# Optimization experiments

Hardware: AMD Instinct MI355X
Metric: run time of the kernel (lower is better)

Reference implementation:

```python
import jax, jax.numpy as jnp
import numpy as np

D_MODEL = 1024
N_HEADS = 16
LN_EPS = 1e-6  # flax LayerNorm default

def setup_inputs() -> dict:
    key = jax.random.key(0)
    k1, k2, k3 = jax.random.split(key, 3)
    B, S = 2, 2048
    x = jax.random.normal(k1, (B, S, D_MODEL), dtype=jnp.float32)
    W_qkv = jax.random.normal(k2, (D_MODEL, 3 * D_MODEL), dtype=jnp.float32) / np.sqrt(D_MODEL)
    W_out = jax.random.normal(k3, (D_MODEL, D_MODEL), dtype=jnp.float32) / np.sqrt(D_MODEL)
    q_scale = jnp.ones((D_MODEL,), dtype=jnp.float32)
    k_scale = jnp.ones((D_MODEL,), dtype=jnp.float32)
    return {"x": x, "W_qkv": W_qkv, "q_scale": q_scale, "k_scale": k_scale, "W_out": W_out}

def _layernorm(t, scale):
    mu = jnp.mean(t, axis=-1, keepdims=True)
    var = jnp.var(t, axis=-1, keepdims=True)
    return (t - mu) * jax.lax.rsqrt(var + LN_EPS) * scale

def reference(x, W_qkv, q_scale, k_scale, W_out):
    B, S, D = x.shape
    H = N_HEADS
    Hd = D // H
    # fused QKV projection (no bias)
    qkv = jnp.einsum('bsd,de->bse', x, W_qkv)
    q, k, v = jnp.split(qkv, 3, axis=-1)
    # QK-LayerNorm over full d_model (before head split), scale only
    q = _layernorm(q, q_scale)
    k = _layernorm(k, k_scale)
    # split heads: [b, s, h, hd]
    q = q.reshape(B, S, H, Hd)
    k = k.reshape(B, S, H, Hd)
    v = v.reshape(B, S, H, Hd)
    # eager attention with causal mask
    scores = jnp.einsum('bshd,bthd->bhst', q / jnp.sqrt(Hd).astype(q.dtype), k)  # [b,h,s,t]
    future = jnp.triu(jnp.ones((S, S), dtype=bool), 1)  # True on strictly-future positions
    scores = jnp.where(future[None, None, :, :], jnp.finfo(scores.dtype).min, scores)
    attn = jax.nn.softmax(scores, axis=-1)
    ctx = jnp.einsum('bhst,bthd->bshd', attn, v)
    out = jnp.einsum('bsd,de->bse', ctx.reshape(B, S, D), W_out)
    return out
```

## Files before the change

kernel.cpp:

```cpp
#include <hip/hip_runtime.h>
#include <cstdint>
#include <cstddef>

typedef __attribute__((ext_vector_type(8))) short short8;
typedef __attribute__((ext_vector_type(4))) float floatx4;

__device__ __forceinline__ float bf2f(unsigned short u) {
  union { unsigned int i; float f; } c; c.i = ((unsigned int)u) << 16; return c.f;
}
__device__ __forceinline__ unsigned short f2bf(float f) {
  union { float f; unsigned int i; } c; c.f = f;
  unsigned int r = c.i + 0x7fffu + ((c.i >> 16) & 1u);
  return (unsigned short)(r >> 16);
}
__device__ __forceinline__ unsigned int fbits(float f) {
  union { float f; unsigned int i; } c; c.f = f; return c.i;
}

__device__ __forceinline__ void glds16(const unsigned short* g, unsigned short* l) {
  __builtin_amdgcn_global_load_lds((const __attribute__((address_space(1))) void*)g,
                                   (__attribute__((address_space(3))) void*)l, 16, 0, 0);
}

__device__ __forceinline__ void tr_tile(const float* __restrict__ in,
                                        unsigned short* __restrict__ out,
                                        int R, int C, int bx, int by, int tid,
                                        unsigned short (*t)[33]) {
  const int cx = tid & 31, rl = tid >> 5;
#pragma unroll
  for (int i = 0; i < 4; ++i)
    t[rl + i * 8][cx] = f2bf(in[(size_t)(by * 32 + rl + i * 8) * C + bx * 32 + cx]);
  __syncthreads();
  const int oc = by * 32 + cx;
#pragma unroll
  for (int i = 0; i < 4; ++i)
    out[(size_t)(bx * 32 + rl + i * 8) * R + oc] = t[cx][rl + i * 8];
}

__global__ __launch_bounds__(256) void k_prep(const float* __restrict__ x,
                                              const float* __restrict__ Wq,
                                              const float* __restrict__ Wo,
                                              unsigned short* __restrict__ x_bf,
                                              unsigned short* __restrict__ WTq,
                                              unsigned short* __restrict__ WTo) {
  __shared__ unsigned short t[32][33];
  const int bid = blockIdx.x, tid = threadIdx.x;
  if (bid < 3072) {
    tr_tile(Wq, WTq, 1024, 3072, bid % 96, bid / 96, tid, t);
  } else if (bid < 4096) {
    int v = bid - 3072;
    tr_tile(Wo, WTo, 1024, 1024, v & 31, v >> 5, tid, t);
  } else {
    int i = (bid - 4096) * 256 + tid;
    float4 v = ((const float4*)x)[i];
    ushort4 o = { f2bf(v.x), f2bf(v.y), f2bf(v.z), f2bf(v.w) };
    ((ushort4*)x_bf)[i] = o;
  }
}

template <int MT, bool F32OUT>
__global__ __launch_bounds__(256) void k_gemm_bt(const unsigned short* __restrict__ A,
                                                 const unsigned short* __restrict__ BT,
                                                 void* __restrict__ Cout,
                                                 int M, int N, int K) {
  constexpr int NI = MT / 32;
  __shared__ unsigned short As[MT * 32];
  __shared__ unsigned short Bs[128 * 32];
  const int bm = blockIdx.x * MT, bn = blockIdx.y * 128;
  const int tid = threadIdx.x;
  const int wave = tid >> 6, lane = tid & 63;
  const int wm = (wave & 1) * (MT / 2), wn = (wave >> 1) * 64;
  const int lrow = lane & 15, lgrp = lane >> 4;
  floatx4 acc[NI][4] = {};

  const int lr4 = lane >> 2, lc8 = (lane & 3) * 8;
  const int br0 = wave * 32;
  const unsigned short* Bg0 = BT + (size_t)(bn + br0 + lr4) * K + lc8;
  const unsigned short* Bg1 = BT + (size_t)(bn + br0 + 16 + lr4) * K + lc8;
  unsigned short* lB0 = &Bs[br0 * 32];
  unsigned short* lB1 = &Bs[(br0 + 16) * 32];
  const int ar0 = wave * (MT / 4);
  const unsigned short* Ag0 = A + (size_t)(bm + ar0 + lr4) * K + lc8;
  const unsigned short* Ag1 = A + (size_t)(bm + ar0 + 16 + lr4) * K + lc8;
  unsigned short* lA0 = &As[ar0 * 32];
  unsigned short* lA1 = &As[(ar0 + 16) * 32];

  for (int k0 = 0; k0 < K; k0 += 32) {
    glds16(Ag0 + k0, lA0);
    if (MT == 128) glds16(Ag1 + k0, lA1);
    glds16(Bg0 + k0, lB0);
    glds16(Bg1 + k0, lB1);
    __syncthreads();
    short8 a[NI], bfr[4];
#pragma unroll
    for (int i = 0; i < NI; ++i)
      a[i] = *(const short8*)&As[(wm + i * 16 + lrow) * 32 + lgrp * 8];
#pragma unroll
    for (int j = 0; j < 4; ++j)
      bfr[j] = *(const short8*)&Bs[(wn + j * 16 + lrow) * 32 + lgrp * 8];
#pragma unroll
    for (int i = 0; i < NI; ++i)
#pragma unroll
      for (int j = 0; j < 4; ++j)
        acc[i][j] = __builtin_amdgcn_mfma_f32_16x16x32_bf16(a[i], bfr[j], acc[i][j], 0, 0, 0);
    __syncthreads();
  }
#pragma unroll
  for (int i = 0; i < NI; ++i)
#pragma unroll
    for (int j = 0; j < 4; ++j)
#pragma unroll
      for (int r = 0; r < 4; ++r) {
        int m = bm + wm + i * 16 + lgrp * 4 + r;
        int n = bn + wn + j * 16 + lrow;
        if (F32OUT)
          ((float*)Cout)[(size_t)m * N + n] = acc[i][j][r];
        else
          ((unsigned short*)Cout)[(size_t)m * N + n] = f2bf(acc[i][j][r]);
      }
}

__global__ __launch_bounds__(256) void k_lnv(const unsigned short* __restrict__ qkv,
                                             const float* __restrict__ q_scale,
                                             const float* __restrict__ k_scale,
                                             unsigned short* __restrict__ q_n,
                                             unsigned short* __restrict__ k_n,
                                             unsigned short* __restrict__ VT) {
  const int bid = blockIdx.x, tid = threadIdx.x;
  if (bid < 4096) {
    const int tok = bid;
    const int wave = tid >> 6, lane = tid & 63;
    __shared__ float red[2][4];
    const unsigned short* row = qkv + (size_t)tok * 3072;
#pragma unroll
    for (int seg = 0; seg < 2; ++seg) {
      const unsigned short* p  = row + seg * 1024;
      const float* sc = seg ? k_scale : q_scale;
      unsigned short* outp = (seg ? k_n : q_n) + (size_t)tok * 1024;
      ushort4 u = *(const ushort4*)&p[tid * 4];
      float xv[4] = { bf2f(u.x), bf2f(u.y), bf2f(u.z), bf2f(u.w) };
      float sum = xv[0] + xv[1] + xv[2] + xv[3];
      float sq  = xv[0]*xv[0] + xv[1]*xv[1] + xv[2]*xv[2] + xv[3]*xv[3];
      for (int off = 32; off; off >>= 1) {
        sum += __shfl_down(sum, off, 64);
        sq  += __shfl_down(sq,  off, 64);
      }
      if (lane == 0) { red[0][wave] = sum; red[1][wave] = sq; }
      __syncthreads();
      sum = red[0][0] + red[0][1] + red[0][2] + red[0][3];
      sq  = red[1][0] + red[1][1] + red[1][2] + red[1][3];
      __syncthreads();
      float mean = sum * (1.0f / 1024.0f);
      float var  = sq * (1.0f / 1024.0f) - mean * mean;
      float rstd = rsqrtf(var + 1e-6f);
      if (seg == 0) rstd *= 0.18033688011112042f;
      float4 su = *(const float4*)&sc[tid * 4];
      ushort4 o;
      o.x = f2bf((xv[0] - mean) * rstd * su.x);
      o.y = f2bf((xv[1] - mean) * rstd * su.y);
      o.z = f2bf((xv[2] - mean) * rstd * su.z);
      o.w = f2bf((xv[3] - mean) * rstd * su.w);
      *(ushort4*)&outp[tid * 4] = o;
    }
  } else {
    __shared__ unsigned short t[32][33];
    const int v = bid - 4096;
    const int bh = v & 31, b = bh >> 4, h = bh & 15;
    const int sy = (v >> 5) & 63, hx = v >> 11;
    const int cx = tid & 31, rl = tid >> 5;
#pragma unroll
    for (int i = 0; i < 4; ++i)
      t[rl + i * 8][cx] =
        qkv[(size_t)(b * 2048 + sy * 32 + rl + i * 8) * 3072 + 2048 + h * 64 + hx * 32 + cx];
    __syncthreads();
#pragma unroll
    for (int i = 0; i < 4; ++i)
      VT[((size_t)bh * 64 + hx * 32 + rl + i * 8) * 2048 + sy * 32 + cx] = t[cx][rl + i * 8];
  }
}


#define KS_STRIDE 72
#define VS_STRIDE 136
#define PS_STRIDE 40

template <bool MASKED>
__device__ __forceinline__ void attn_step(int t0, int q0, int wave,
    const short8 (&qa)[4][2],
    const unsigned short* Ks, const unsigned short* Vs, unsigned short* Psw,
    floatx4 (&o)[4][4], float (&l)[4], int lrow, int lgrp) {
  const int tw = t0 + wave * 32;
#pragma unroll
  for (int tb = 0; tb < 2; ++tb) {
    short8 kb0 = *(const short8*)&Ks[(wave * 32 + tb * 16 + lrow) * KS_STRIDE + lgrp * 8];
    short8 kb1 = *(const short8*)&Ks[(wave * 32 + tb * 16 + lrow) * KS_STRIDE + 32 + lgrp * 8];
#pragma unroll
    for (int qb = 0; qb < 4; ++qb) {
      floatx4 st = {};
      st = __builtin_amdgcn_mfma_f32_16x16x32_bf16(kb0, qa[qb][0], st, 0, 0, 0);
      st = __builtin_amdgcn_mfma_f32_16x16x32_bf16(kb1, qa[qb][1], st, 0, 0, 0);
      float p0 = exp2f(st[0]), p1 = exp2f(st[1]);
      float p2 = exp2f(st[2]), p3 = exp2f(st[3]);
      if (MASKED) {
        const int qcol = q0 + qb * 16 + lrow;
        const int tbase = tw + tb * 16 + lgrp * 4;
        p0 = (tbase     <= qcol) ? p0 : 0.0f;
        p1 = (tbase + 1 <= qcol) ? p1 : 0.0f;
        p2 = (tbase + 2 <= qcol) ? p2 : 0.0f;
        p3 = (tbase + 3 <= qcol) ? p3 : 0.0f;
      }
      l[qb] += (p0 + p1) + (p2 + p3);
      uint2 pu;
      pu.x = (fbits(p0) >> 16) | (fbits(p1) & 0xFFFF0000u);
      pu.y = (fbits(p2) >> 16) | (fbits(p3) & 0xFFFF0000u);
      *(uint2*)&Psw[(qb * 16 + lrow) * PS_STRIDE + tb * 16 + lgrp * 4] = pu;
    }
  }
  short8 vb[4];
#pragma unroll
  for (int hb = 0; hb < 4; ++hb)
    vb[hb] = *(const short8*)&Vs[(hb * 16 + lrow) * VS_STRIDE + wave * 32 + lgrp * 8];
#pragma unroll
  for (int qb = 0; qb < 4; ++qb) {
    short8 pa = *(const short8*)&Psw[(qb * 16 + lrow) * PS_STRIDE + lgrp * 8];
#pragma unroll
    for (int hb = 0; hb < 4; ++hb)
      o[qb][hb] = __builtin_amdgcn_mfma_f32_16x16x32_bf16(pa, vb[hb], o[qb][hb], 0, 0, 0);
  }
}

__global__ __launch_bounds__(256) void k_flash(const unsigned short* __restrict__ q_n,
                                               const unsigned short* __restrict__ k_n,
                                               const unsigned short* __restrict__ VT,
                                               unsigned short* __restrict__ ctx) {
  const int S = 2048, D = 1024;
  const int bh = blockIdx.x, b = bh >> 4, h = bh & 15;
  const int qt = 31 - (int)blockIdx.y;
  const int q0 = qt * 64;
  const int tid = threadIdx.x, wave = tid >> 6, lane = tid & 63;
  const int lrow = lane & 15, lgrp = lane >> 4;

  __shared__ __align__(16) unsigned char smem[56320];
  unsigned short* Ks  = (unsigned short*)smem;
  unsigned short* Vs  = (unsigned short*)(smem + 18432);
  unsigned short* Psw = (unsigned short*)(smem + 35840) + wave * 64 * PS_STRIDE;
  float* buf0 = (float*)smem;
  float* buf1 = (float*)(smem + 16384);
  float* Lbuf = (float*)(smem + 35840);

  const unsigned short* kg = k_n + (size_t)(b * S) * D + h * 64;
  const unsigned short* vg = VT + (size_t)bh * 64 * S;
  const int ksr = tid >> 3, ksc = (tid & 7) * 8;
  const int vsr = tid >> 4, vsc = (tid & 15) * 8;

  short8 qa[4][2];
#pragma unroll
  for (int qb = 0; qb < 4; ++qb) {
    const unsigned short* qp = q_n + (size_t)(b * S + q0 + qb * 16 + lrow) * D + h * 64;
    qa[qb][0] = *(const short8*)(qp + lgrp * 8);
    qa[qb][1] = *(const short8*)(qp + 32 + lgrp * 8);
  }
  floatx4 o[4][4] = {};
  float l[4] = {};

  const int tend = q0 + 64;
  for (int t0 = 0; t0 < tend; t0 += 128) {
#pragma unroll
    for (int j = 0; j < 4; ++j) {
      int r = ksr + j * 32;
      *(int4*)&Ks[r * KS_STRIDE + ksc] = *(const int4*)(kg + (size_t)(t0 + r) * D + ksc);
    }
#pragma unroll
    for (int j = 0; j < 4; ++j) {
      int r = vsr + j * 16;
      *(int4*)&Vs[r * VS_STRIDE + vsc] = *(const int4*)(vg + (size_t)r * S + t0 + vsc);
    }
    __syncthreads();
    if (t0 + 128 <= q0)
      attn_step<false>(t0, q0, wave, qa, Ks, Vs, Psw, o, l, lrow, lgrp);
    else
      attn_step<true>(t0, q0, wave, qa, Ks, Vs, Psw, o, l, lrow, lgrp);
    __syncthreads();
  }

#pragma unroll
  for (int qb = 0; qb < 4; ++qb) {
    l[qb] += __shfl_xor(l[qb], 16, 64);
    l[qb] += __shfl_xor(l[qb], 32, 64);
  }
  if (lane < 16) {
#pragma unroll
    for (int qb = 0; qb < 4; ++qb)
      Lbuf[wave * 64 + qb * 16 + lrow] = l[qb];
  }
  if (wave == 2 || wave == 3) {
    float* bf = (wave == 2) ? buf0 : buf1;
#pragma unroll
    for (int qb = 0; qb < 4; ++qb)
#pragma unroll
      for (int hb = 0; hb < 4; ++hb)
#pragma unroll
        for (int r = 0; r < 4; ++r)
          bf[(qb * 16 + lgrp * 4 + r) * 64 + hb * 16 + lrow] = o[qb][hb][r];
  }
  __syncthreads();
  if (wave == 0 || wave == 1) {
    float* bf = (wave == 0) ? buf0 : buf1;
#pragma unroll
    for (int qb = 0; qb < 4; ++qb)
#pragma unroll
      for (int hb = 0; hb < 4; ++hb)
#pragma unroll
        for (int r = 0; r < 4; ++r)
          o[qb][hb][r] += bf[(qb * 16 + lgrp * 4 + r) * 64 + hb * 16 + lrow];
    if (wave == 1)
#pragma unroll
      for (int qb = 0; qb < 4; ++qb)
#pragma unroll
        for (int hb = 0; hb < 4; ++hb)
#pragma unroll
          for (int r = 0; r < 4; ++r)
            buf1[(qb * 16 + lgrp * 4 + r) * 64 + hb * 16 + lrow] = o[qb][hb][r];
  }
  __syncthreads();
  if (wave == 0) {
#pragma unroll
    for (int qb = 0; qb < 4; ++qb)
#pragma unroll
      for (int hb = 0; hb < 4; ++hb)
#pragma unroll
        for (int r = 0; r < 4; ++r) {
          float v = o[qb][hb][r] + buf1[(qb * 16 + lgrp * 4 + r) * 64 + hb * 16 + lrow];
          buf0[(qb * 16 + lgrp * 4 + r) * 64 + hb * 16 + lrow] = v;
        }
  }
  __syncthreads();
  {
    const int q = tid >> 2, cb = tid & 3;
    float lq = Lbuf[q] + Lbuf[64 + q] + Lbuf[128 + q] + Lbuf[192 + q];
    float inv = 1.0f / lq;
    const float* src = buf0 + q * 64 + cb * 16;
    short8 w0, w1;
#pragma unroll
    for (int i = 0; i < 8; ++i) ((unsigned short*)&w0)[i] = f2bf(src[i] * inv);
#pragma unroll
    for (int i = 0; i < 8; ++i) ((unsigned short*)&w1)[i] = f2bf(src[8 + i] * inv);
    unsigned short* op = ctx + (size_t)(b * S + q0 + q) * D + h * 64 + cb * 16;
    *(short8*)op = w0;
    *(short8*)(op + 8) = w1;
  }
}

extern "C" void kernel_launch(void* const* d_in, const int* in_sizes, int n_in,
                              void* d_out, int out_size, void* d_ws, size_t ws_size,
                              hipStream_t stream) {
  const float* x       = (const float*)d_in[0];
  const float* W_qkv   = (const float*)d_in[1];
  const float* q_scale = (const float*)d_in[2];
  const float* k_scale = (const float*)d_in[3];
  const float* W_out   = (const float*)d_in[4];
  float* out = (float*)d_out;
  char* ws = (char*)d_ws;
  unsigned short* WT_qkv = (unsigned short*)(ws + 0);
  unsigned short* WT_out = (unsigned short*)(ws + 6291456);
  unsigned short* qkv    = (unsigned short*)(ws + 8388608);
  unsigned short* q_nb   = (unsigned short*)(ws + 33554432);
  unsigned short* k_nb   = (unsigned short*)(ws + 41943040);
  unsigned short* VT     = (unsigned short*)(ws + 50331648);
  unsigned short* x_bf   = (unsigned short*)(ws + 58720256);
  unsigned short* ctx    = qkv;

  k_prep<<<8192, 256, 0, stream>>>(x, W_qkv, W_out, x_bf, WT_qkv, WT_out);
  k_gemm_bt<128, false><<<dim3(32, 24), 256, 0, stream>>>(x_bf, WT_qkv, qkv, 4096, 3072, 1024);
  k_lnv<<<8192, 256, 0, stream>>>(qkv, q_scale, k_scale, q_nb, k_nb, VT);
  k_flash<<<dim3(32, 32), 256, 0, stream>>>(q_nb, k_nb, VT, ctx);
  k_gemm_bt<64, true><<<dim3(64, 8), 256, 0, stream>>>(ctx, WT_out, out, 4096, 1024, 1024);
}
```

Measured before the change: 203.8 us.

## Split flash waves over query and key halves; double K-step in GEMM loop

The flash-attention kernel now assigns each wave a 32-query by 64-key sub-tile, where before each wave handled all 64 queries against 32 keys. This cuts the cross-wave output reduction from a four-way LDS tree to a single two-way merge, skips the idle key half on the last diagonal tile, and writes the context directly from registers. The GEMM kernel loads two 32-wide K slices per barrier pair, halving synchronisations at the cost of twice the LDS footprint. Risks include different register pressure and direct strided bf16 stores to the context buffer.

```diff
diff --git a/kernel.cpp b/kernel.cpp
--- a/kernel.cpp
+++ b/kernel.cpp
@@ -64,8 +64,8 @@
                                                  void* __restrict__ Cout,
                                                  int M, int N, int K) {
   constexpr int NI = MT / 32;
-  __shared__ unsigned short As[MT * 32];
-  __shared__ unsigned short Bs[128 * 32];
+  __shared__ unsigned short As[2][MT * 32];
+  __shared__ unsigned short Bs[2][128 * 32];
   const int bm = blockIdx.x * MT, bn = blockIdx.y * 128;
   const int tid = threadIdx.x;
   const int wave = tid >> 6, lane = tid & 63;
@@ -77,32 +77,35 @@
   const int br0 = wave * 32;
   const unsigned short* Bg0 = BT + (size_t)(bn + br0 + lr4) * K + lc8;
   const unsigned short* Bg1 = BT + (size_t)(bn + br0 + 16 + lr4) * K + lc8;
-  unsigned short* lB0 = &Bs[br0 * 32];
-  unsigned short* lB1 = &Bs[(br0 + 16) * 32];
   const int ar0 = wave * (MT / 4);
   const unsigned short* Ag0 = A + (size_t)(bm + ar0 + lr4) * K + lc8;
   const unsigned short* Ag1 = A + (size_t)(bm + ar0 + 16 + lr4) * K + lc8;
-  unsigned short* lA0 = &As[ar0 * 32];
-  unsigned short* lA1 = &As[(ar0 + 16) * 32];
-
-  for (int k0 = 0; k0 < K; k0 += 32) {
-    glds16(Ag0 + k0, lA0);
-    if (MT == 128) glds16(Ag1 + k0, lA1);
-    glds16(Bg0 + k0, lB0);
-    glds16(Bg1 + k0, lB1);
-    __syncthreads();
-    short8 a[NI], bfr[4];
-#pragma unroll
-    for (int i = 0; i < NI; ++i)
-      a[i] = *(const short8*)&As[(wm + i * 16 + lrow) * 32 + lgrp * 8];
-#pragma unroll
-    for (int j = 0; j < 4; ++j)
-      bfr[j] = *(const short8*)&Bs[(wn + j * 16 + lrow) * 32 + lgrp * 8];
-#pragma unroll
-    for (int i = 0; i < NI; ++i)
+
+  for (int k0 = 0; k0 < K; k0 += 64) {
+#pragma unroll
+    for (int u = 0; u < 2; ++u) {
+      const int ko = k0 + u * 32;
+      glds16(Ag0 + ko, &As[u][ar0 * 32]);
+      if (MT == 128) glds16(Ag1 + ko, &As[u][(ar0 + 16) * 32]);
+      glds16(Bg0 + ko, &Bs[u][br0 * 32]);
+      glds16(Bg1 + ko, &Bs[u][(br0 + 16) * 32]);
+    }
+    __syncthreads();
+#pragma unroll
+    for (int u = 0; u < 2; ++u) {
+      short8 a[NI], bfr[4];
+#pragma unroll
+      for (int i = 0; i < NI; ++i)
+        a[i] = *(const short8*)&As[u][(wm + i * 16 + lrow) * 32 + lgrp * 8];
 #pragma unroll
       for (int j = 0; j < 4; ++j)
-        acc[i][j] = __builtin_amdgcn_mfma_f32_16x16x32_bf16(a[i], bfr[j], acc[i][j], 0, 0, 0);
+        bfr[j] = *(const short8*)&Bs[u][(wn + j * 16 + lrow) * 32 + lgrp * 8];
+#pragma unroll
+      for (int i = 0; i < NI; ++i)
+#pragma unroll
+        for (int j = 0; j < 4; ++j)
+          acc[i][j] = __builtin_amdgcn_mfma_f32_16x16x32_bf16(a[i], bfr[j], acc[i][j], 0, 0, 0);
+    }
     __syncthreads();
   }
 #pragma unroll
@@ -182,28 +185,28 @@
 
 #define KS_STRIDE 72
 #define VS_STRIDE 136
-#define PS_STRIDE 40
+#define PS_STRIDE 72
 
 template <bool MASKED>
-__device__ __forceinline__ void attn_step(int t0, int q0, int wave,
-    const short8 (&qa)[4][2],
+__device__ __forceinline__ void attn_step(int t0, int q0, int wq, int wt,
+    const short8 (&qa)[2][2],
     const unsigned short* Ks, const unsigned short* Vs, unsigned short* Psw,
-    floatx4 (&o)[4][4], float (&l)[4], int lrow, int lgrp) {
-  const int tw = t0 + wave * 32;
-#pragma unroll
-  for (int tb = 0; tb < 2; ++tb) {
-    short8 kb0 = *(const short8*)&Ks[(wave * 32 + tb * 16 + lrow) * KS_STRIDE + lgrp * 8];
-    short8 kb1 = *(const short8*)&Ks[(wave * 32 + tb * 16 + lrow) * KS_STRIDE + 32 + lgrp * 8];
-#pragma unroll
-    for (int qb = 0; qb < 4; ++qb) {
+    floatx4 (&o)[2][4], float (&l)[2], int lrow, int lgrp) {
+  const int twbase = wt * 64;
+#pragma unroll
+  for (int tb = 0; tb < 4; ++tb) {
+    short8 kb0 = *(const short8*)&Ks[(twbase + tb * 16 + lrow) * KS_STRIDE + lgrp * 8];
+    short8 kb1 = *(const short8*)&Ks[(twbase + tb * 16 + lrow) * KS_STRIDE + 32 + lgrp * 8];
+#pragma unroll
+    for (int qb = 0; qb < 2; ++qb) {
       floatx4 st = {};
       st = __builtin_amdgcn_mfma_f32_16x16x32_bf16(kb0, qa[qb][0], st, 0, 0, 0);
       st = __builtin_amdgcn_mfma_f32_16x16x32_bf16(kb1, qa[qb][1], st, 0, 0, 0);
       float p0 = exp2f(st[0]), p1 = exp2f(st[1]);
       float p2 = exp2f(st[2]), p3 = exp2f(st[3]);
       if (MASKED) {
-        const int qcol = q0 + qb * 16 + lrow;
-        const int tbase = tw + tb * 16 + lgrp * 4;
+        const int qcol = q0 + wq * 32 + qb * 16 + lrow;
+        const int tbase = t0 + twbase + tb * 16 + lgrp * 4;
         p0 = (tbase     <= qcol) ? p0 : 0.0f;
         p1 = (tbase + 1 <= qcol) ? p1 : 0.0f;
         p2 = (tbase + 2 <= qcol) ? p2 : 0.0f;
@@ -216,16 +219,16 @@
       *(uint2*)&Psw[(qb * 16 + lrow) * PS_STRIDE + tb * 16 + lgrp * 4] = pu;
     }
   }
-  short8 vb[4];
-#pragma unroll
-  for (int hb = 0; hb < 4; ++hb)
-    vb[hb] = *(const short8*)&Vs[(hb * 16 + lrow) * VS_STRIDE + wave * 32 + lgrp * 8];
-#pragma unroll
-  for (int qb = 0; qb < 4; ++qb) {
-    short8 pa = *(const short8*)&Psw[(qb * 16 + lrow) * PS_STRIDE + lgrp * 8];
-#pragma unroll
-    for (int hb = 0; hb < 4; ++hb)
-      o[qb][hb] = __builtin_amdgcn_mfma_f32_16x16x32_bf16(pa, vb[hb], o[qb][hb], 0, 0, 0);
+#pragma unroll
+  for (int kk = 0; kk < 2; ++kk) {
+    short8 pa0 = *(const short8*)&Psw[lrow * PS_STRIDE + kk * 32 + lgrp * 8];
+    short8 pa1 = *(const short8*)&Psw[(16 + lrow) * PS_STRIDE + kk * 32 + lgrp * 8];
+#pragma unroll
+    for (int hb = 0; hb < 4; ++hb) {
+      short8 vb = *(const short8*)&Vs[(hb * 16 + lrow) * VS_STRIDE + twbase + kk * 32 + lgrp * 8];
+      o[0][hb] = __builtin_amdgcn_mfma_f32_16x16x32_bf16(pa0, vb, o[0][hb], 0, 0, 0);
+      o[1][hb] = __builtin_amdgcn_mfma_f32_16x16x32_bf16(pa1, vb, o[1][hb], 0, 0, 0);
+    }
   }
 }
 
@@ -238,30 +241,31 @@
   const int qt = 31 - (int)blockIdx.y;
   const int q0 = qt * 64;
   const int tid = threadIdx.x, wave = tid >> 6, lane = tid & 63;
+  const int wq = wave >> 1, wt = wave & 1;
   const int lrow = lane & 15, lgrp = lane >> 4;
 
-  __shared__ __align__(16) unsigned char smem[56320];
+  __shared__ __align__(16) unsigned char smem[54272];
   unsigned short* Ks  = (unsigned short*)smem;
   unsigned short* Vs  = (unsigned short*)(smem + 18432);
-  unsigned short* Psw = (unsigned short*)(smem + 35840) + wave * 64 * PS_STRIDE;
-  float* buf0 = (float*)smem;
-  float* buf1 = (float*)(smem + 16384);
-  float* Lbuf = (float*)(smem + 35840);
+  unsigned short* Psw = (unsigned short*)(smem + 35840) + wave * 32 * PS_STRIDE;
+  float* buf  = (float*)smem;
+  float* Lbuf = (float*)(smem + 17408);
 
   const unsigned short* kg = k_n + (size_t)(b * S) * D + h * 64;
   const unsigned short* vg = VT + (size_t)bh * 64 * S;
   const int ksr = tid >> 3, ksc = (tid & 7) * 8;
   const int vsr = tid >> 4, vsc = (tid & 15) * 8;
 
-  short8 qa[4][2];
-#pragma unroll
-  for (int qb = 0; qb < 4; ++qb) {
-    const unsigned short* qp = q_n + (size_t)(b * S + q0 + qb * 16 + lrow) * D + h * 64;
+  short8 qa[2][2];
+#pragma unroll
+  for (int qb = 0; qb < 2; ++qb) {
+    const unsigned short* qp =
+        q_n + (size_t)(b * S + q0 + wq * 32 + qb * 16 + lrow) * D + h * 64;
     qa[qb][0] = *(const short8*)(qp + lgrp * 8);
     qa[qb][1] = *(const short8*)(qp + 32 + lgrp * 8);
   }
-  floatx4 o[4][4] = {};
-  float l[4] = {};
+  floatx4 o[2][4] = {};
+  float l[2] = {};
 
   const int tend = q0 + 64;
   for (int t0 = 0; t0 < tend; t0 += 128) {
@@ -276,78 +280,58 @@
       *(int4*)&Vs[r * VS_STRIDE + vsc] = *(const int4*)(vg + (size_t)r * S + t0 + vsc);
     }
     __syncthreads();
-    if (t0 + 128 <= q0)
-      attn_step<false>(t0, q0, wave, qa, Ks, Vs, Psw, o, l, lrow, lgrp);
-    else
-      attn_step<true>(t0, q0, wave, qa, Ks, Vs, Psw, o, l, lrow, lgrp);
-    __syncthreads();
-  }
-
-#pragma unroll
-  for (int qb = 0; qb < 4; ++qb) {
+    const bool half = (tend - t0) < 128;
+    if (!(half && wt == 1)) {
+      if (t0 + 128 <= q0)
+        attn_step<false>(t0, q0, wq, wt, qa, Ks, Vs, Psw, o, l, lrow, lgrp);
+      else
+        attn_step<true>(t0, q0, wq, wt, qa, Ks, Vs, Psw, o, l, lrow, lgrp);
+    }
+    __syncthreads();
+  }
+
+#pragma unroll
+  for (int qb = 0; qb < 2; ++qb) {
     l[qb] += __shfl_xor(l[qb], 16, 64);
     l[qb] += __shfl_xor(l[qb], 32, 64);
   }
-  if (lane < 16) {
-#pragma unroll
-    for (int qb = 0; qb < 4; ++qb)
-      Lbuf[wave * 64 + qb * 16 + lrow] = l[qb];
-  }
-  if (wave == 2 || wave == 3) {
-    float* bf = (wave == 2) ? buf0 : buf1;
-#pragma unroll
-    for (int qb = 0; qb < 4; ++qb)
+  if (wt == 1) {
+    if (lane < 16) {
+      Lbuf[wq * 32 + lrow]      = l[0];
+      Lbuf[wq * 32 + 16 + lrow] = l[1];
+    }
+    float* bf = buf + wq * 32 * 68;
+#pragma unroll
+    for (int qb = 0; qb < 2; ++qb)
 #pragma unroll
       for (int hb = 0; hb < 4; ++hb)
 #pragma unroll
         for (int r = 0; r < 4; ++r)
-          bf[(qb * 16 + lgrp * 4 + r) * 64 + hb * 16 + lrow] = o[qb][hb][r];
+          bf[(qb * 16 + lgrp * 4 + r) * 68 + hb * 16 + lrow] = o[qb][hb][r];
   }
   __syncthreads();
-  if (wave == 0 || wave == 1) {
-    float* bf = (wave == 0) ? buf0 : buf1;
-#pragma unroll
-    for (int qb = 0; qb < 4; ++qb)
+  if (wt == 0) {
+    float* bf = buf + wq * 32 * 68;
+#pragma unroll
+    for (int qb = 0; qb < 2; ++qb) {
+      l[qb] += Lbuf[wq * 32 + qb * 16 + lrow];
 #pragma unroll
       for (int hb = 0; hb < 4; ++hb)
 #pragma unroll
         for (int r = 0; r < 4; ++r)
-          o[qb][hb][r] += bf[(qb * 16 + lgrp * 4 + r) * 64 + hb * 16 + lrow];
-    if (wave == 1)
-#pragma unroll
-      for (int qb = 0; qb < 4; ++qb)
+          o[qb][hb][r] += bf[(qb * 16 + lgrp * 4 + r) * 68 + hb * 16 + lrow];
+    }
+    unsigned short* op = ctx + (size_t)(b * S + q0 + wq * 32) * D + h * 64;
+#pragma unroll
+    for (int qb = 0; qb < 2; ++qb)
+#pragma unroll
+      for (int r = 0; r < 4; ++r) {
+        float inv = 1.0f / __shfl(l[qb], lgrp * 4 + r, 64);
+        int row = qb * 16 + lgrp * 4 + r;
 #pragma unroll
         for (int hb = 0; hb < 4; ++hb)
-#pragma unroll
-          for (int r = 0; r < 4; ++r)
-            buf1[(qb * 16 + lgrp * 4 + r) * 64 + hb * 16 + lrow] = o[qb][hb][r];
-  }
-  __syncthreads();
-  if (wave == 0) {
-#pragma unroll
-    for (int qb = 0; qb < 4; ++qb)
-#pragma unroll
-      for (int hb = 0; hb < 4; ++hb)
-#pragma unroll
-        for (int r = 0; r < 4; ++r) {
-          float v = o[qb][hb][r] + buf1[(qb * 16 + lgrp * 4 + r) * 64 + hb * 16 + lrow];
-          buf0[(qb * 16 + lgrp * 4 + r) * 64 + hb * 16 + lrow] = v;
-        }
-  }
-  __syncthreads();
-  {
-    const int q = tid >> 2, cb = tid & 3;
-    float lq = Lbuf[q] + Lbuf[64 + q] + Lbuf[128 + q] + Lbuf[192 + q];
-    float inv = 1.0f / lq;
-    const float* src = buf0 + q * 64 + cb * 16;
-    short8 w0, w1;
-#pragma unroll
-    for (int i = 0; i < 8; ++i) ((unsigned short*)&w0)[i] = f2bf(src[i] * inv);
-#pragma unroll
-    for (int i = 0; i < 8; ++i) ((unsigned short*)&w1)[i] = f2bf(src[8 + i] * inv);
-    unsigned short* op = ctx + (size_t)(b * S + q0 + q) * D + h * 64 + cb * 16;
-    *(short8*)op = w0;
-    *(short8*)(op + 8) = w1;
+          op[(size_t)row * D + hb * 16 + lrow] = f2bf(o[qb][hb][r] * inv);
+      }
   }
 }
 
```

Result: faster. 192.2 us (-5.7%).
